# Performance work log

Measured on AMD Instinct MI355X. Metric: run time of the kernel, lower is better.

## Reference

```python
import jax, jax.numpy as jnp
import numpy as np

D_MODEL = 768
HEADS = 12
HEAD_DIM = D_MODEL // HEADS


def setup_inputs() -> dict:
    key = jax.random.key(0)
    ks = jax.random.split(key, 5)
    B, L = 4, 2048
    x = jax.random.normal(ks[0], (B, L, D_MODEL), dtype=jnp.float32)
    # torch nn.Linear init scale ~ 1/sqrt(fan_in); use small random weights
    s = 1.0 / np.sqrt(D_MODEL)
    W_qkv = jax.random.uniform(ks[1], (D_MODEL, 3 * D_MODEL), jnp.float32, -s, s)
    b_qkv = jax.random.uniform(ks[2], (3 * D_MODEL,), jnp.float32, -s, s)
    W_out = jax.random.uniform(ks[3], (D_MODEL, D_MODEL), jnp.float32, -s, s)
    b_out = jax.random.uniform(ks[4], (D_MODEL,), jnp.float32, -s, s)
    return {"x": x, "W_qkv": W_qkv, "b_qkv": b_qkv, "W_out": W_out, "b_out": b_out}


def reference(x, W_qkv, b_qkv, W_out, b_out):
    B, L, D = x.shape
    scale = jnp.sqrt(jnp.float32(HEAD_DIM))
    # qkv projection: [B, L, 3*D] -> [3, B, heads, L, head_dim]
    qkv = (x @ W_qkv + b_qkv).reshape(B, L, 3, HEADS, HEAD_DIM)
    qkv = jnp.transpose(qkv, (2, 0, 3, 1, 4))
    q, k, v = qkv[0], qkv[1], qkv[2]
    # full materialized attention, no mask
    scores = jnp.einsum("bhld,bhmd->bhlm", q, k) / scale  # [B, H, L, L]
    attn = jax.nn.softmax(scores, axis=-1)
    out = jnp.einsum("bhlm,bhmd->bhld", attn, v)  # [B, H, L, head_dim]
    out = jnp.transpose(out, (0, 2, 1, 3)).reshape(B, L, D)
    return out @ W_out + b_out
```

## Files before the change

kernel.cpp:

```cpp
#include <hip/hip_runtime.h>
#include <cmath>

typedef __bf16 bf16_t;
typedef __bf16 bf16x8 __attribute__((ext_vector_type(8)));
typedef __bf16 bf16x4 __attribute__((ext_vector_type(4)));
typedef short s16x4 __attribute__((ext_vector_type(4)));
typedef float f32x4 __attribute__((ext_vector_type(4)));

#define MFMA(a, b, c) __builtin_amdgcn_mfma_f32_16x16x32_bf16((a), (b), (c), 0, 0, 0)
#if __has_builtin(__builtin_amdgcn_mfma_f32_16x16x16_bf16)
#define MFMA16(a, b, c) __builtin_amdgcn_mfma_f32_16x16x16_bf16((a), (b), (c), 0, 0, 0)
#else
#define MFMA16(a, b, c)                                                              \
  __builtin_amdgcn_mfma_f32_16x16x16bf16_1k(__builtin_bit_cast(s16x4, (bf16x4)(a)), \
                                            __builtin_bit_cast(s16x4, (bf16x4)(b)), (c), 0, 0, 0)
#endif

#define EXP2(x) __builtin_amdgcn_exp2f(x)

static constexpr int D = 768;
static constexpr int L = 2048;
static constexpr int NB = 4;
static constexpr int NH = 12;
static constexpr int HD = 64;
static constexpr int M = 8192;
static constexpr int NQKV = 2304;
#define QSCALE 0.18033688011112042f

__device__ __forceinline__ void glds16(const bf16_t* g, bf16_t* l) {
  __builtin_amdgcn_global_load_lds((const __attribute__((address_space(1))) void*)g,
                                   (__attribute__((address_space(3))) void*)l, 16, 0, 0);
}

__global__ __launch_bounds__(256) void cvt_bf16_kernel(const float* __restrict__ in,
                                                       bf16_t* __restrict__ out, int n8) {
  int g = blockIdx.x * 256 + threadIdx.x;
  if (g >= n8) return;
  const float4* p = (const float4*)in + (size_t)g * 2;
  float4 a = p[0], b = p[1];
  bf16x8 v = {(__bf16)a.x, (__bf16)a.y, (__bf16)a.z, (__bf16)a.w,
              (__bf16)b.x, (__bf16)b.y, (__bf16)b.z, (__bf16)b.w};
  *(bf16x8*)(out + (size_t)g * 8) = v;
}

__global__ __launch_bounds__(256) void transpose_cvt_kernel(const float* __restrict__ in,
                                                            bf16_t* __restrict__ out,
                                                            int rows, int cols) {
  __shared__ float t[32][33];
  int c0 = blockIdx.x * 32, r0 = blockIdx.y * 32;
  int tx = threadIdx.x, ty = threadIdx.y;
  for (int i = ty; i < 32; i += 8) t[i][tx] = in[(size_t)(r0 + i) * cols + c0 + tx];
  __syncthreads();
  for (int i = ty; i < 32; i += 8) out[(size_t)(c0 + i) * rows + r0 + tx] = (__bf16)t[tx][i];
}

__global__ __launch_bounds__(256) void gemm_qkv_kernel(const bf16_t* __restrict__ A,
                                                       const bf16_t* __restrict__ Bt,
                                                       const float* __restrict__ bias,
                                                       bf16_t* __restrict__ Qo,
                                                       bf16_t* __restrict__ Ko,
                                                       bf16_t* __restrict__ Vto) {
  __shared__ __align__(16) bf16_t As[128 * 32];
  __shared__ __align__(16) bf16_t Bs[128 * 32];
  const int tid = threadIdx.x;
  const int wave = tid >> 6, lane = tid & 63;
  const int quad = lane >> 4, l16 = lane & 15;
  const int wm = (wave >> 1) * 64, wn = (wave & 1) * 64;
  const int tm = blockIdx.x * 128, tn = blockIdx.y * 128;
  const int lr = tid >> 2, lc = (tid & 3) * 8;
  const bf16_t* Ag = A + (size_t)(tm + lr) * D + lc;
  const bf16_t* Bg = Bt + (size_t)(tn + lr) * D + lc;
  bf16_t* lA0 = &As[wave * 512];
  bf16_t* lA1 = &As[2048 + wave * 512];
  bf16_t* lB0 = &Bs[wave * 512];
  bf16_t* lB1 = &Bs[2048 + wave * 512];
  f32x4 acc[4][4] = {};
  for (int kt = 0; kt < D; kt += 32) {
    __syncthreads();
    glds16(Ag + kt, lA0);
    glds16(Ag + (size_t)64 * D + kt, lA1);
    glds16(Bg + kt, lB0);
    glds16(Bg + (size_t)64 * D + kt, lB1);
    __syncthreads();
    bf16x8 af[4], bfr[4];
#pragma unroll
    for (int i = 0; i < 4; i++) af[i] = *(const bf16x8*)&As[(wm + i * 16 + l16) * 32 + quad * 8];
#pragma unroll
    for (int j = 0; j < 4; j++) bfr[j] = *(const bf16x8*)&Bs[(wn + j * 16 + l16) * 32 + quad * 8];
#pragma unroll
    for (int i = 0; i < 4; i++)
#pragma unroll
      for (int j = 0; j < 4; j++) acc[i][j] = MFMA(af[i], bfr[j], acc[i][j]);
  }
#pragma unroll
  for (int i = 0; i < 4; i++)
#pragma unroll
    for (int j = 0; j < 4; j++) {
      int n = tn + wn + j * 16 + l16;
      float bn = bias[n];
      int which = n / 768, rem = n - which * 768;
      int h = rem >> 6, d = rem & 63;
      int m0 = tm + wm + i * 16 + quad * 4;
      int b0 = m0 >> 11, l0 = m0 & 2047;
      int bh = b0 * NH + h;
      if (which == 2) {
        int blk = (l0 & 2047) >> 6, l6 = l0 & 63;
        int lp = (((l6 >> 2) & 3) * 16) | ((l6 >> 4) * 4);
        bf16x4 w;
#pragma unroll
        for (int r2 = 0; r2 < 4; r2++) w[r2] = (__bf16)(acc[i][j][r2] + bn);
        *(bf16x4*)&Vto[(((size_t)bh * (L / 64) + blk) * HD + d) * 64 + lp] = w;
      } else if (which == 0) {
#pragma unroll
        for (int r2 = 0; r2 < 4; r2++)
          Qo[((size_t)bh * L + l0 + r2) * HD + d] = (__bf16)((acc[i][j][r2] + bn) * QSCALE);
      } else {
#pragma unroll
        for (int r2 = 0; r2 < 4; r2++)
          Ko[((size_t)bh * L + l0 + r2) * HD + d] = (__bf16)(acc[i][j][r2] + bn);
      }
    }
}

__global__ __launch_bounds__(256) void attn_kernel(const bf16_t* __restrict__ Q,
                                                   const bf16_t* __restrict__ K,
                                                   const bf16_t* __restrict__ Vt,
                                                   bf16_t* __restrict__ O) {
  __shared__ __align__(16) bf16_t Ks[64][72];
  __shared__ __align__(16) bf16_t Vs[64][72];
  const int tid = threadIdx.x;
  const int wave = tid >> 6, lane = tid & 63;
  const int quad = lane >> 4, l16 = lane & 15;
  const int bh = blockIdx.y;
  const int q0 = blockIdx.x * 128 + wave * 32;
  const bf16_t* Kb = K + (size_t)bh * L * HD;
  const bf16_t* Vb = Vt + (size_t)bh * HD * L;
  bf16x8 bq[2][2];
#pragma unroll
  for (int g = 0; g < 2; g++) {
    const bf16_t* Qp = Q + ((size_t)bh * L + q0 + g * 16 + l16) * HD + quad * 8;
    bq[g][0] = *(const bf16x8*)Qp;
    bq[g][1] = *(const bf16x8*)(Qp + 32);
  }
  f32x4 oacc[2][4] = {};
  float lacc[2] = {0.f, 0.f};
  const int st = tid >> 3, sc = (tid & 7) * 8;
  const bf16_t* pK0 = Kb + (size_t)st * HD + sc;
  const bf16_t* pK1 = Kb + (size_t)(st + 32) * HD + sc;
  const bf16_t* pV0 = Vb + (size_t)st * 64 + sc;
  const bf16_t* pV1 = Vb + (size_t)(st + 32) * 64 + sc;
  bf16x8 pk0 = *(const bf16x8*)pK0;
  bf16x8 pk1 = *(const bf16x8*)pK1;
  bf16x8 pv0 = *(const bf16x8*)pV0;
  bf16x8 pv1 = *(const bf16x8*)pV1;
  for (int j = 0; j < L / 64; j++) {
    __syncthreads();
    *(bf16x8*)&Ks[st][sc] = pk0;
    *(bf16x8*)&Ks[st + 32][sc] = pk1;
    *(bf16x8*)&Vs[st][sc] = pv0;
    *(bf16x8*)&Vs[st + 32][sc] = pv1;
    __syncthreads();
    if (j + 1 < L / 64) {
      pK0 += 64 * HD;
      pK1 += 64 * HD;
      pV0 += HD * 64;
      pV1 += HD * 64;
      pk0 = *(const bf16x8*)pK0;
      pk1 = *(const bf16x8*)pK1;
      pv0 = *(const bf16x8*)pV0;
      pv1 = *(const bf16x8*)pV1;
    }
    f32x4 s[2][4];
#pragma unroll
    for (int fn = 0; fn < 4; fn++) {
      bf16x8 ak0 = *(const bf16x8*)&Ks[fn * 16 + l16][quad * 8];
      bf16x8 ak1 = *(const bf16x8*)&Ks[fn * 16 + l16][32 + quad * 8];
#pragma unroll
      for (int g = 0; g < 2; g++) {
        f32x4 z = {};
        z = MFMA(ak0, bq[g][0], z);
        s[g][fn] = MFMA(ak1, bq[g][1], z);
      }
    }
    bf16x4 pb[2][4];
#pragma unroll
    for (int g = 0; g < 2; g++)
#pragma unroll
      for (int fn = 0; fn < 4; fn++) {
        float e0 = EXP2(s[g][fn][0]), e1 = EXP2(s[g][fn][1]);
        float e2 = EXP2(s[g][fn][2]), e3 = EXP2(s[g][fn][3]);
        lacc[g] += (e0 + e1) + (e2 + e3);
        bf16x4 w = {(__bf16)e0, (__bf16)e1, (__bf16)e2, (__bf16)e3};
        pb[g][fn] = w;
      }
#pragma unroll
    for (int fd = 0; fd < 4; fd++)
#pragma unroll
      for (int t = 0; t < 2; t++) {
        bf16x8 av2 = *(const bf16x8*)&Vs[fd * 16 + l16][quad * 16 + t * 8];
        bf16x4 av0 = {av2[0], av2[1], av2[2], av2[3]};
        bf16x4 av1 = {av2[4], av2[5], av2[6], av2[7]};
#pragma unroll
        for (int g = 0; g < 2; g++) {
          oacc[g][fd] = MFMA16(av0, pb[g][2 * t], oacc[g][fd]);
          oacc[g][fd] = MFMA16(av1, pb[g][2 * t + 1], oacc[g][fd]);
        }
      }
  }
  const int b = bh / NH, h = bh - b * NH;
#pragma unroll
  for (int g = 0; g < 2; g++) {
    float ls = lacc[g];
    ls += __shfl_xor(ls, 16, 64);
    ls += __shfl_xor(ls, 32, 64);
    float rinv = 1.f / ls;
    int row = q0 + g * 16 + l16;
    bf16_t* Op = O + ((size_t)(b * L + row)) * D + h * HD;
#pragma unroll
    for (int fd = 0; fd < 4; fd++) {
      bf16x4 w;
#pragma unroll
      for (int r = 0; r < 4; r++) w[r] = (__bf16)(oacc[g][fd][r] * rinv);
      *(bf16x4*)(Op + fd * 16 + quad * 4) = w;
    }
  }
}

__global__ __launch_bounds__(256) void gemm_out_kernel(const bf16_t* __restrict__ A,
                                                       const bf16_t* __restrict__ Bt,
                                                       const float* __restrict__ bias,
                                                       float* __restrict__ Cg) {
  __shared__ __align__(16) bf16_t As[128 * 32];
  __shared__ __align__(16) bf16_t Bs[64 * 32];
  const int tid = threadIdx.x;
  const int wave = tid >> 6, lane = tid & 63;
  const int quad = lane >> 4, l16 = lane & 15;
  const int wm = (wave >> 1) * 64, wn = (wave & 1) * 32;
  const int tm = blockIdx.x * 128, tn = blockIdx.y * 64;
  const int lr = tid >> 2, lc = (tid & 3) * 8;
  const bf16_t* Ag = A + (size_t)(tm + lr) * D + lc;
  const bf16_t* Bg = Bt + (size_t)(tn + (lr & 63)) * D + lc;
  bf16_t* lA0 = &As[wave * 512];
  bf16_t* lA1 = &As[2048 + wave * 512];
  bf16_t* lB0 = &Bs[wave * 512];
  f32x4 acc[4][2] = {};
  for (int kt = 0; kt < D; kt += 32) {
    __syncthreads();
    glds16(Ag + kt, lA0);
    glds16(Ag + (size_t)64 * D + kt, lA1);
    glds16(Bg + kt, lB0);
    __syncthreads();
    bf16x8 af[4], bfr[2];
#pragma unroll
    for (int i = 0; i < 4; i++) af[i] = *(const bf16x8*)&As[(wm + i * 16 + l16) * 32 + quad * 8];
#pragma unroll
    for (int j = 0; j < 2; j++) bfr[j] = *(const bf16x8*)&Bs[(wn + j * 16 + l16) * 32 + quad * 8];
#pragma unroll
    for (int i = 0; i < 4; i++)
#pragma unroll
      for (int j = 0; j < 2; j++) acc[i][j] = MFMA(af[i], bfr[j], acc[i][j]);
  }
#pragma unroll
  for (int i = 0; i < 4; i++)
#pragma unroll
    for (int j = 0; j < 2; j++) {
      int n = tn + wn + j * 16 + l16;
      float bn = bias[n];
#pragma unroll
      for (int r2 = 0; r2 < 4; r2++) {
        int m = tm + wm + i * 16 + quad * 4 + r2;
        Cg[(size_t)m * D + n] = acc[i][j][r2] + bn;
      }
    }
}

extern "C" void kernel_launch(void* const* d_in, const int* in_sizes, int n_in,
                              void* d_out, int out_size, void* d_ws, size_t ws_size,
                              hipStream_t stream) {
  const float* x = (const float*)d_in[0];
  const float* Wqkv = (const float*)d_in[1];
  const float* bqkv = (const float*)d_in[2];
  const float* Wout = (const float*)d_in[3];
  const float* bout = (const float*)d_in[4];
  float* out = (float*)d_out;

  bf16_t* xb = (bf16_t*)d_ws;
  bf16_t* wqT = xb + (size_t)M * D;
  bf16_t* woT = wqT + (size_t)NQKV * D;
  bf16_t* Qb = woT + (size_t)D * D;
  bf16_t* Kb = Qb + (size_t)M * D;
  bf16_t* Vtb = Kb + (size_t)M * D;
  bf16_t* Ob = Vtb + (size_t)M * D;

  cvt_bf16_kernel<<<(M * D / 8 + 255) / 256, 256, 0, stream>>>(x, xb, M * D / 8);
  transpose_cvt_kernel<<<dim3(NQKV / 32, D / 32), dim3(32, 8), 0, stream>>>(Wqkv, wqT, D, NQKV);
  transpose_cvt_kernel<<<dim3(D / 32, D / 32), dim3(32, 8), 0, stream>>>(Wout, woT, D, D);
  gemm_qkv_kernel<<<dim3(M / 128, NQKV / 128), 256, 0, stream>>>(xb, wqT, bqkv, Qb, Kb, Vtb);
  attn_kernel<<<dim3(L / 128, NB * NH), 256, 0, stream>>>(Qb, Kb, Vtb, Ob);
  gemm_out_kernel<<<dim3(M / 128, D / 64), 256, 0, stream>>>(Ob, woT, bout, out);
}
```

Baseline: 225.6 us.

## Use 16x16x32 MFMA for PV, deepen QKV GEMM k-step, remap attention blocks per XCD

The attention PV product switches from pairs of 16x16x16 MFMAs to a single 16x16x32 MFMA. To support this, the V-transpose layout written by the QKV GEMM is permuted so each lane reads one contiguous 8-element chunk. The QKV GEMM now loads two 32-wide K slices per barrier pair, halving the synchronisations per K. The attention grid is flattened to 1D, and heads are assigned by XCD index so each XCD's L2 holds the K/V of only six heads; this raises shared memory use in the GEMM.

After: 231.5 us. +2.6%, slower.

```diff
diff --git a/kernel.cpp b/kernel.cpp
--- a/kernel.cpp
+++ b/kernel.cpp
@@ -4,18 +4,9 @@
 typedef __bf16 bf16_t;
 typedef __bf16 bf16x8 __attribute__((ext_vector_type(8)));
 typedef __bf16 bf16x4 __attribute__((ext_vector_type(4)));
-typedef short s16x4 __attribute__((ext_vector_type(4)));
 typedef float f32x4 __attribute__((ext_vector_type(4)));
 
 #define MFMA(a, b, c) __builtin_amdgcn_mfma_f32_16x16x32_bf16((a), (b), (c), 0, 0, 0)
-#if __has_builtin(__builtin_amdgcn_mfma_f32_16x16x16_bf16)
-#define MFMA16(a, b, c) __builtin_amdgcn_mfma_f32_16x16x16_bf16((a), (b), (c), 0, 0, 0)
-#else
-#define MFMA16(a, b, c)                                                              \
-  __builtin_amdgcn_mfma_f32_16x16x16bf16_1k(__builtin_bit_cast(s16x4, (bf16x4)(a)), \
-                                            __builtin_bit_cast(s16x4, (bf16x4)(b)), (c), 0, 0, 0)
-#endif
-
 #define EXP2(x) __builtin_amdgcn_exp2f(x)
 
 static constexpr int D = 768;
@@ -60,8 +51,8 @@
                                                        bf16_t* __restrict__ Qo,
                                                        bf16_t* __restrict__ Ko,
                                                        bf16_t* __restrict__ Vto) {
-  __shared__ __align__(16) bf16_t As[128 * 32];
-  __shared__ __align__(16) bf16_t Bs[128 * 32];
+  __shared__ __align__(16) bf16_t As[2][128 * 32];
+  __shared__ __align__(16) bf16_t Bs[2][128 * 32];
   const int tid = threadIdx.x;
   const int wave = tid >> 6, lane = tid & 63;
   const int quad = lane >> 4, l16 = lane & 15;
@@ -70,27 +61,32 @@
   const int lr = tid >> 2, lc = (tid & 3) * 8;
   const bf16_t* Ag = A + (size_t)(tm + lr) * D + lc;
   const bf16_t* Bg = Bt + (size_t)(tn + lr) * D + lc;
-  bf16_t* lA0 = &As[wave * 512];
-  bf16_t* lA1 = &As[2048 + wave * 512];
-  bf16_t* lB0 = &Bs[wave * 512];
-  bf16_t* lB1 = &Bs[2048 + wave * 512];
   f32x4 acc[4][4] = {};
-  for (int kt = 0; kt < D; kt += 32) {
-    __syncthreads();
-    glds16(Ag + kt, lA0);
-    glds16(Ag + (size_t)64 * D + kt, lA1);
-    glds16(Bg + kt, lB0);
-    glds16(Bg + (size_t)64 * D + kt, lB1);
-    __syncthreads();
-    bf16x8 af[4], bfr[4];
-#pragma unroll
-    for (int i = 0; i < 4; i++) af[i] = *(const bf16x8*)&As[(wm + i * 16 + l16) * 32 + quad * 8];
-#pragma unroll
-    for (int j = 0; j < 4; j++) bfr[j] = *(const bf16x8*)&Bs[(wn + j * 16 + l16) * 32 + quad * 8];
-#pragma unroll
-    for (int i = 0; i < 4; i++)
-#pragma unroll
-      for (int j = 0; j < 4; j++) acc[i][j] = MFMA(af[i], bfr[j], acc[i][j]);
+  for (int kt = 0; kt < D; kt += 64) {
+    __syncthreads();
+    glds16(Ag + kt, &As[0][wave * 512]);
+    glds16(Ag + (size_t)64 * D + kt, &As[0][2048 + wave * 512]);
+    glds16(Ag + kt + 32, &As[1][wave * 512]);
+    glds16(Ag + (size_t)64 * D + kt + 32, &As[1][2048 + wave * 512]);
+    glds16(Bg + kt, &Bs[0][wave * 512]);
+    glds16(Bg + (size_t)64 * D + kt, &Bs[0][2048 + wave * 512]);
+    glds16(Bg + kt + 32, &Bs[1][wave * 512]);
+    glds16(Bg + (size_t)64 * D + kt + 32, &Bs[1][2048 + wave * 512]);
+    __syncthreads();
+#pragma unroll
+    for (int kh = 0; kh < 2; kh++) {
+      bf16x8 af[4], bfr[4];
+#pragma unroll
+      for (int i = 0; i < 4; i++)
+        af[i] = *(const bf16x8*)&As[kh][(wm + i * 16 + l16) * 32 + quad * 8];
+#pragma unroll
+      for (int j = 0; j < 4; j++)
+        bfr[j] = *(const bf16x8*)&Bs[kh][(wn + j * 16 + l16) * 32 + quad * 8];
+#pragma unroll
+      for (int i = 0; i < 4; i++)
+#pragma unroll
+        for (int j = 0; j < 4; j++) acc[i][j] = MFMA(af[i], bfr[j], acc[i][j]);
+    }
   }
 #pragma unroll
   for (int i = 0; i < 4; i++)
@@ -104,12 +100,16 @@
       int b0 = m0 >> 11, l0 = m0 & 2047;
       int bh = b0 * NH + h;
       if (which == 2) {
-        int blk = (l0 & 2047) >> 6, l6 = l0 & 63;
-        int lp = (((l6 >> 2) & 3) * 16) | ((l6 >> 4) * 4);
-        bf16x4 w;
-#pragma unroll
-        for (int r2 = 0; r2 < 4; r2++) w[r2] = (__bf16)(acc[i][j][r2] + bn);
-        *(bf16x4*)&Vto[(((size_t)bh * (L / 64) + blk) * HD + d) * 64 + lp] = w;
+        int blk = l0 >> 6;
+        int v6 = l0 & 63;
+        int t = v6 >> 5, w = v6 & 31;
+        int lo = (w < 16);
+        int q = (lo ? w : w - 16) >> 2;
+        int p0 = t * 32 + q * 8 + (lo ? 0 : 4);
+        bf16x4 wv;
+#pragma unroll
+        for (int r2 = 0; r2 < 4; r2++) wv[r2] = (__bf16)(acc[i][j][r2] + bn);
+        *(bf16x4*)&Vto[(((size_t)bh * (L / 64) + blk) * HD + d) * 64 + p0] = wv;
       } else if (which == 0) {
 #pragma unroll
         for (int r2 = 0; r2 < 4; r2++)
@@ -131,8 +131,10 @@
   const int tid = threadIdx.x;
   const int wave = tid >> 6, lane = tid & 63;
   const int quad = lane >> 4, l16 = lane & 15;
-  const int bh = blockIdx.y;
-  const int q0 = blockIdx.x * 128 + wave * 32;
+  const int id = blockIdx.x;
+  const int xcd = id & 7, slot = id >> 3;
+  const int bh = xcd * 6 + (slot % 6);
+  const int q0 = (slot / 6) * 128 + wave * 32;
   const bf16_t* Kb = K + (size_t)bh * L * HD;
   const bf16_t* Vb = Vt + (size_t)bh * HD * L;
   bf16x8 bq[2][2];
@@ -182,29 +184,27 @@
         s[g][fn] = MFMA(ak1, bq[g][1], z);
       }
     }
-    bf16x4 pb[2][4];
+    bf16x8 pq[2][2];
 #pragma unroll
     for (int g = 0; g < 2; g++)
 #pragma unroll
-      for (int fn = 0; fn < 4; fn++) {
-        float e0 = EXP2(s[g][fn][0]), e1 = EXP2(s[g][fn][1]);
-        float e2 = EXP2(s[g][fn][2]), e3 = EXP2(s[g][fn][3]);
-        lacc[g] += (e0 + e1) + (e2 + e3);
-        bf16x4 w = {(__bf16)e0, (__bf16)e1, (__bf16)e2, (__bf16)e3};
-        pb[g][fn] = w;
+      for (int t = 0; t < 2; t++) {
+        float e0 = EXP2(s[g][2 * t][0]), e1 = EXP2(s[g][2 * t][1]);
+        float e2 = EXP2(s[g][2 * t][2]), e3 = EXP2(s[g][2 * t][3]);
+        float e4 = EXP2(s[g][2 * t + 1][0]), e5 = EXP2(s[g][2 * t + 1][1]);
+        float e6 = EXP2(s[g][2 * t + 1][2]), e7 = EXP2(s[g][2 * t + 1][3]);
+        lacc[g] += ((e0 + e1) + (e2 + e3)) + ((e4 + e5) + (e6 + e7));
+        bf16x8 w = {(__bf16)e0, (__bf16)e1, (__bf16)e2, (__bf16)e3,
+                    (__bf16)e4, (__bf16)e5, (__bf16)e6, (__bf16)e7};
+        pq[g][t] = w;
       }
 #pragma unroll
     for (int fd = 0; fd < 4; fd++)
 #pragma unroll
       for (int t = 0; t < 2; t++) {
-        bf16x8 av2 = *(const bf16x8*)&Vs[fd * 16 + l16][quad * 16 + t * 8];
-        bf16x4 av0 = {av2[0], av2[1], av2[2], av2[3]};
-        bf16x4 av1 = {av2[4], av2[5], av2[6], av2[7]};
-#pragma unroll
-        for (int g = 0; g < 2; g++) {
-          oacc[g][fd] = MFMA16(av0, pb[g][2 * t], oacc[g][fd]);
-          oacc[g][fd] = MFMA16(av1, pb[g][2 * t + 1], oacc[g][fd]);
-        }
+        bf16x8 av = *(const bf16x8*)&Vs[fd * 16 + l16][t * 32 + quad * 8];
+#pragma unroll
+        for (int g = 0; g < 2; g++) oacc[g][fd] = MFMA(av, pq[g][t], oacc[g][fd]);
       }
   }
   const int b = bh / NH, h = bh - b * NH;
@@ -296,6 +296,6 @@
   transpose_cvt_kernel<<<dim3(NQKV / 32, D / 32), dim3(32, 8), 0, stream>>>(Wqkv, wqT, D, NQKV);
   transpose_cvt_kernel<<<dim3(D / 32, D / 32), dim3(32, 8), 0, stream>>>(Wout, woT, D, D);
   gemm_qkv_kernel<<<dim3(M / 128, NQKV / 128), 256, 0, stream>>>(xb, wqT, bqkv, Qb, Kb, Vtb);
-  attn_kernel<<<dim3(L / 128, NB * NH), 256, 0, stream>>>(Qb, Kb, Vtb, Ob);
+  attn_kernel<<<768, 256, 0, stream>>>(Qb, Kb, Vtb, Ob);
   gemm_out_kernel<<<dim3(M / 128, D / 64), 256, 0, stream>>>(Ob, woT, bout, out);
 }
```
